# Kernel tuning notes

Measured on AMD Instinct MI355X. Metric: run time of the kernel, lower is better.

## Reference

```python
import jax, jax.numpy as jnp
import numpy as np

B, N, DIM = 2, 4096, 1024
HEADS, DH, W = 16, 64, 512
INNER = int(DIM * 2 * 4 / 3)  # 2730 (GEGLU FeedForward, mult=4)


def setup_inputs() -> dict:
    key = jax.random.key(0)
    ks = jax.random.split(key, 6)
    rn = lambda k, shape, sc: jax.random.normal(k, shape, jnp.float32) * sc
    return {
        "x": rn(ks[0], (B, N, DIM), 1.0),
        "ln1_w": jnp.ones((DIM,), jnp.float32),
        "ln1_b": jnp.zeros((DIM,), jnp.float32),
        "w_qkv": rn(ks[1], (DIM, 3 * HEADS * DH), 0.02),
        "w_out": rn(ks[2], (HEADS * DH, DIM), 0.02),
        "ln2_w": jnp.ones((DIM,), jnp.float32),
        "w_ff1": rn(ks[3], (DIM, 2 * INNER), 0.02),
        "w_ff2": rn(ks[4], (INNER, DIM), 0.02),
    }


def _layernorm(x, w, b=None, eps=1e-5):
    m = x.mean(-1, keepdims=True)
    v = x.var(-1, keepdims=True)
    y = (x - m) * jax.lax.rsqrt(v + eps) * w
    return y + b if b is not None else y


def _rotary_freqs(n, d):
    inv = 1.0 / (10000.0 ** (jnp.arange(0, d, 2, dtype=jnp.float32) / d))
    f = jnp.arange(n, dtype=jnp.float32)[:, None] * inv[None, :]  # [n, d/2]
    return jnp.concatenate([f, f], axis=-1)  # [n, d]


def _rotate_half(x):
    x1, x2 = jnp.split(x, 2, axis=-1)
    return jnp.concatenate([-x2, x1], axis=-1)


def _apply_rotary(x, freqs):
    return x * jnp.cos(freqs) + _rotate_half(x) * jnp.sin(freqs)


def reference(x, ln1_w, ln1_b, w_qkv, w_out, ln2_w, w_ff1, w_ff2):
    # ---- LocalMHA (prenorm, causal windowed attention, look_backward=1) ----
    h = _layernorm(x, ln1_w, ln1_b)
    qkv = h @ w_qkv  # [b, n, 3*h*d]
    q, k, v = jnp.split(qkv, 3, axis=-1)
    to_heads = lambda t: t.reshape(B, N, HEADS, DH).transpose(0, 2, 1, 3)  # [b,h,n,d]
    q, k, v = map(to_heads, (q, k, v))

    freqs = _rotary_freqs(N, DH)  # [n, d]
    q = _apply_rotary(q, freqs)
    k = _apply_rotary(k, freqs)
    q = q * (DH ** -0.5)

    nw = N // W
    bq = q.reshape(B, HEADS, nw, W, DH)
    bk = k.reshape(B, HEADS, nw, W, DH)
    bv = v.reshape(B, HEADS, nw, W, DH)

    def look_back(t):  # prepend previous window (zeros for first window)
        prev = jnp.concatenate([jnp.zeros_like(t[:, :, :1]), t[:, :, :-1]], axis=2)
        return jnp.concatenate([prev, t], axis=3)  # [b,h,nw,2w,d]

    kk, vv = look_back(bk), look_back(bv)

    tq = jnp.arange(N).reshape(nw, W)
    tprev = jnp.concatenate([jnp.full((1, W), -1, tq.dtype), tq[:-1]], axis=0)
    tk = jnp.concatenate([tprev, tq], axis=1)  # [nw, 2w]
    mask = (tq[:, :, None] >= tk[:, None, :]) & (tk[:, None, :] >= 0)  # causal + pad

    sim = jnp.einsum('bhnqd,bhnkd->bhnqk', bq, kk)
    sim = jnp.where(mask, sim, jnp.finfo(sim.dtype).min / 2)
    attn = jax.nn.softmax(sim, axis=-1)
    o = jnp.einsum('bhnqk,bhnkd->bhnqd', attn, vv)
    o = o.reshape(B, HEADS, N, DH).transpose(0, 2, 1, 3).reshape(B, N, HEADS * DH)
    x = o @ w_out + x  # residual

    # ---- FeedForward: LN(gamma only) -> GEGLU -> Linear, residual ----
    h = _layernorm(x, ln2_w)
    u = h @ w_ff1
    a, g = jnp.split(u, 2, axis=-1)
    x = (a * jax.nn.gelu(g, approximate=False)) @ w_ff2 + x
    return x
```

## Files before the change

kernel.cpp:

```cpp
#include <hip/hip_runtime.h>
#include <stdint.h>

typedef unsigned short u16;
typedef unsigned int u32;

#define BATCH 2
#define NSEQ  4096
#define DIM   1024
#define HEADS 16
#define DH    64
#define WIN   512
#define INNER 2730
#define ROWS  8192
#define QKV_N 3072
#define FF1_N 5460
#define FF1_NP 5632
#define INNER_P 2816
#define KROT 0.28782313663f

typedef __attribute__((ext_vector_type(8))) short short8;
typedef __attribute__((ext_vector_type(4))) float float4v;

__device__ __forceinline__ float bf2f(u16 u){ union{u32 i;float f;}c; c.i=((u32)u)<<16; return c.f; }
__device__ __forceinline__ u16 f2bf(float f){ union{float f;u32 i;}c; c.f=f; u32 i=c.i;
    return (u16)((i + 0x7FFFu + ((i>>16)&1u))>>16); }

__device__ __forceinline__ float gelu_fast(float g) {
    float t = 0.7978845608f * (g + 0.044715f * g * g * g);
    float th = 1.f - 2.f / (1.f + __expf(2.f * t));
    return 0.5f * g * (1.f + th);
}

__device__ __forceinline__ void gl_lds16(const u16* g, const u16* ldsbase) {
    __builtin_amdgcn_global_load_lds(
        (const __attribute__((address_space(1))) u32*)(uintptr_t)g,
        (__attribute__((address_space(3))) u32*)(uintptr_t)ldsbase,
        16, 0, 0);
}

__device__ __forceinline__ int ff1_src(int n, bool& ok) {
    int t = n >> 7, m = n & 127, j = m >> 4, l = m & 15;
    int p = t * 64 + ((j >> 1) << 4) + l;
    ok = (p < INNER);
    return (j & 1) ? (INNER + p) : p;
}

template <bool REMAP>
__global__ __launch_bounds__(256) void wtrans_kernel(const float* __restrict__ w, u16* __restrict__ wt,
                                                     int K0, int N0, int K1, int N1) {
    __shared__ float tile[32][33];
    int kt = blockIdx.x, nt = blockIdx.y;
    int tx = threadIdx.x & 31, ty = threadIdx.x >> 5;
    int nl = nt * 32 + tx;
    bool ok = (nl < N1);
    int sc = nl;
    if (REMAP) { bool v; sc = ff1_src(nl < N1 ? nl : 0, v); ok = ok && v; }
    else ok = ok && (nl < N0);
#pragma unroll
    for (int yy = 0; yy < 4; yy++) {
        int k = kt*32 + ty + yy*8;
        tile[ty+yy*8][tx] = (k < K0 && ok) ? w[(size_t)k*N0 + sc] : 0.f;
    }
    __syncthreads();
#pragma unroll
    for (int yy = 0; yy < 4; yy++) {
        int n = nt*32 + ty + yy*8, k = kt*32 + tx;
        if (n < N1 && k < K1) wt[(size_t)n*K1 + k] = f2bf(tile[tx][ty+yy*8]);
    }
}

__global__ __launch_bounds__(256) void ln_kernel(const float* __restrict__ x,
                                                 const float* __restrict__ w,
                                                 const float* __restrict__ b,
                                                 u16* __restrict__ out) {
    int row = blockIdx.x;
    const float* xr = x + (size_t)row * DIM;
    int t = threadIdx.x;
    float v[4];
    float s = 0.f, s2 = 0.f;
#pragma unroll
    for (int i = 0; i < 4; i++) {
        float f = xr[t + 256 * i];
        v[i] = f; s += f; s2 += f * f;
    }
#pragma unroll
    for (int off = 32; off; off >>= 1) { s += __shfl_xor(s, off); s2 += __shfl_xor(s2, off); }
    __shared__ float ls[10];
    int wave = t >> 6, lane = t & 63;
    if (lane == 0) { ls[wave] = s; ls[4 + wave] = s2; }
    __syncthreads();
    if (t == 0) {
        float ts  = ls[0] + ls[1] + ls[2] + ls[3];
        float ts2 = ls[4] + ls[5] + ls[6] + ls[7];
        float mean = ts * (1.f / DIM);
        float var  = ts2 * (1.f / DIM) - mean * mean;
        ls[8] = mean; ls[9] = 1.f / sqrtf(var + 1e-5f);
    }
    __syncthreads();
    float mean = ls[8], inv = ls[9];
    u16* orow = out + (size_t)row * DIM;
#pragma unroll
    for (int i = 0; i < 4; i++) {
        int c = t + 256 * i;
        float y = (v[i] - mean) * inv * w[c];
        if (b) y += b[c];
        orow[c] = f2bf(y);
    }
}

template <int MODE>
__global__ __launch_bounds__(512, 2) void gemm256(const u16* __restrict__ A,
                                                  const u16* __restrict__ Bt,
                                                  void* __restrict__ Cv,
                                                  int N, int K) {
    extern __shared__ u16 lds[];
    u16* Asm = lds;
    u16* Bsm = lds + 4 * 8192;
    int tiles_n = N >> 8;
    int gs  = tiles_n << 3;
    int gid = blockIdx.x / gs;
    int loc = blockIdx.x % gs;
    int tm = gid * 8 + (loc & 7);
    int tn = loc >> 3;
    int tid = threadIdx.x, wave = tid >> 6, lane = tid & 63;
    int quad = lane >> 4, l15 = lane & 15;
    int wm = wave >> 2, wn = wave & 3;
    int srow = wave * 16 + (lane >> 2);
    int sgrp = (lane & 3) ^ ((srow >> 1) & 3);
    const u16* Ag = A  + (size_t)(tm * 256 + srow) * K + sgrp * 8;
    const u16* Bg = Bt + (size_t)(tn * 256 + srow) * K + sgrp * 8;
    u16* Asw = Asm + wave * 512;
    u16* Bsw = Bsm + wave * 512;
    int rg = (l15 >> 1) & 3;
    int nk = K >> 5;

    float4v acc[8][4];
#pragma unroll
    for (int i = 0; i < 8; i++)
#pragma unroll
        for (int j = 0; j < 4; j++) acc[i][j] = (float4v){0.f, 0.f, 0.f, 0.f};

    auto stage2 = [&](int t, int h) {
        int b = t & 3;
        int k0 = t << 5;
        if (h == 0) {
            gl_lds16(Ag + k0,                   Asw + b * 8192);
            gl_lds16(Ag + (size_t)128 * K + k0, Asw + b * 8192 + 4096);
        } else {
            gl_lds16(Bg + k0,                   Bsw + b * 8192);
            gl_lds16(Bg + (size_t)128 * K + k0, Bsw + b * 8192 + 4096);
        }
    };
    auto ldsA = [&](int t, int i) -> short8 {
        const u16* Ab = Asm + (t & 3) * 8192;
        return *(const short8*)&Ab[(wm*128 + i*16 + l15) * 32 + ((quad ^ rg) * 8)];
    };
    auto ldsB = [&](int t, int j) -> short8 {
        const u16* Bb = Bsm + (t & 3) * 8192;
        return *(const short8*)&Bb[(wn*64 + j*16 + l15) * 32 + ((quad ^ rg) * 8)];
    };

    stage2(0, 0); stage2(0, 1);
    stage2(1, 0); stage2(1, 1);
    stage2(2, 0); stage2(2, 1);
    asm volatile("s_waitcnt vmcnt(8)" ::: "memory");
    __builtin_amdgcn_s_barrier();

    for (int t = 0; t < nk; ++t) {
        short8 af[8], bfr[4];
#pragma unroll
        for (int i = 0; i < 4; i++) af[i] = ldsA(t, i);
#pragma unroll
        for (int j = 0; j < 4; j++) bfr[j] = ldsB(t, j);
        if (t + 3 < nk) stage2(t + 3, 0);
        __builtin_amdgcn_s_barrier();
        asm volatile("s_waitcnt lgkmcnt(0)" ::: "memory");
        __builtin_amdgcn_sched_barrier(0);
        __builtin_amdgcn_s_setprio(1);
#pragma unroll
        for (int i = 0; i < 4; i++)
#pragma unroll
            for (int j = 0; j < 4; j++)
                acc[i][j] = __builtin_amdgcn_mfma_f32_16x16x32_bf16(af[i], bfr[j], acc[i][j], 0, 0, 0);
        __builtin_amdgcn_s_setprio(0);
        __builtin_amdgcn_s_barrier();
#pragma unroll
        for (int i = 4; i < 8; i++) af[i] = ldsA(t, i);
        if (t + 3 < nk) stage2(t + 3, 1);
        __builtin_amdgcn_s_barrier();
        asm volatile("s_waitcnt lgkmcnt(0)" ::: "memory");
        __builtin_amdgcn_sched_barrier(0);
        __builtin_amdgcn_s_setprio(1);
#pragma unroll
        for (int i = 4; i < 8; i++)
#pragma unroll
            for (int j = 0; j < 4; j++)
                acc[i][j] = __builtin_amdgcn_mfma_f32_16x16x32_bf16(af[i], bfr[j], acc[i][j], 0, 0, 0);
        __builtin_amdgcn_s_setprio(0);
        if (t < nk - 1) {
            if (t < nk - 3)       asm volatile("s_waitcnt vmcnt(8)" ::: "memory");
            else if (t == nk - 3) asm volatile("s_waitcnt vmcnt(4)" ::: "memory");
            else                  asm volatile("s_waitcnt vmcnt(0)" ::: "memory");
            __builtin_amdgcn_s_barrier();
        }
    }

    if (MODE == 2) {
        u16* C = (u16*)Cv;
        int sector = tn >> 2;
        if (sector < 2) {
            float inv0 = __expf(-(float)l15 * KROT);
            float inv1 = __expf(-(float)(l15 + 16) * KROT);
            float sc = (sector == 0) ? 0.125f : 1.0f;
#pragma unroll
            for (int i = 0; i < 8; i++) {
#pragma unroll
                for (int r = 0; r < 4; r++) {
                    int row = tm*256 + wm*128 + i*16 + quad*4 + r;
                    float fn = (float)(row & (NSEQ - 1));
                    float s0, c0, s1, c1;
                    __sincosf(fn * inv0, &s0, &c0);
                    __sincosf(fn * inv1, &s1, &c1);
                    float a0 = acc[i][0][r], a1 = acc[i][1][r];
                    float a2 = acc[i][2][r], a3 = acc[i][3][r];
                    size_t base = (size_t)row * N + tn*256 + wn*64 + l15;
                    C[base]      = f2bf((a0*c0 - a2*s0) * sc);
                    C[base + 16] = f2bf((a1*c1 - a3*s1) * sc);
                    C[base + 32] = f2bf((a2*c0 + a0*s0) * sc);
                    C[base + 48] = f2bf((a3*c1 + a1*s1) * sc);
                }
            }
        } else {
#pragma unroll
            for (int i = 0; i < 8; i++)
#pragma unroll
                for (int r = 0; r < 4; r++) {
                    size_t base = (size_t)(tm*256 + wm*128 + i*16 + quad*4 + r) * N + tn*256 + wn*64 + l15;
#pragma unroll
                    for (int j = 0; j < 4; j++) C[base + j*16] = f2bf(acc[i][j][r]);
                }
        }
        return;
    }
    if (MODE == 3) {
        u16* ag = (u16*)Cv;
        int t128 = tn * 2 + (wn >> 1);
        int cb = t128 * 64 + (wn & 1) * 32;
#pragma unroll
        for (int i = 0; i < 8; i++) {
#pragma unroll
            for (int r = 0; r < 4; r++) {
                size_t row = (size_t)(tm*256 + wm*128 + i*16 + quad*4 + r);
#pragma unroll
                for (int jp = 0; jp < 2; jp++) {
                    float a = acc[i][2*jp][r];
                    float g = acc[i][2*jp+1][r];
                    int col = cb + jp*16 + l15;
                    ag[row * INNER_P + col] = f2bf(a * gelu_fast(g));
                }
            }
        }
        return;
    }
}

template <int MODE>
__global__ __launch_bounds__(256) void gemm_tile(const u16* __restrict__ A,
                                                 const u16* __restrict__ Bt,
                                                 const float* __restrict__ resid,
                                                 void* __restrict__ Cv,
                                                 int M, int N, int K) {
    __shared__ u16 As[2][128 * 32];
    __shared__ u16 Bs[2][128 * 32];
    int tiles_n = N >> 7;
    int gs  = tiles_n << 3;
    int gid = blockIdx.x / gs;
    int loc = blockIdx.x % gs;
    int tm = gid * 8 + (loc & 7);
    int tn = loc >> 3;
    int tid = threadIdx.x, wave = tid >> 6, lane = tid & 63;
    int quad = lane >> 4, l15 = lane & 15;
    int wm = wave >> 1, wn = wave & 1;
    int srow = wave * 32 + (lane >> 2);
    int sgrp = (lane & 3) ^ ((srow >> 1) & 3);
    const u16* Ag = A  + (size_t)(tm * 128 + srow) * K + sgrp * 8;
    const u16* Bg = Bt + (size_t)(tn * 128 + srow) * K + sgrp * 8;
    const u16* Alb0 = &As[0][wave * 1024];
    const u16* Blb0 = &Bs[0][wave * 1024];
    const u16* Alb1 = &As[1][wave * 1024];
    const u16* Blb1 = &Bs[1][wave * 1024];
    int rg = (l15 >> 1) & 3;
    float4v acc[4][4];
#pragma unroll
    for (int i = 0; i < 4; i++)
#pragma unroll
        for (int j = 0; j < 4; j++) acc[i][j] = (float4v){0.f, 0.f, 0.f, 0.f};

    gl_lds16(Ag,                Alb0);
    gl_lds16(Ag + (size_t)16*K, Alb0 + 512);
    gl_lds16(Bg,                Blb0);
    gl_lds16(Bg + (size_t)16*K, Blb0 + 512);
    __syncthreads();

    int nk = K >> 5;
    for (int t = 0; t < nk; ++t) {
        int buf = t & 1;
        if (t + 1 < nk) {
            int k0 = (t + 1) << 5;
            const u16* Al = buf ? Alb0 : Alb1;
            const u16* Bl = buf ? Blb0 : Blb1;
            gl_lds16(Ag + k0,                Al);
            gl_lds16(Ag + (size_t)16*K + k0, Al + 512);
            gl_lds16(Bg + k0,                Bl);
            gl_lds16(Bg + (size_t)16*K + k0, Bl + 512);
        }
        const u16* Asb = &As[buf][0];
        const u16* Bsb = &Bs[buf][0];
        short8 af[4], bf[4];
#pragma unroll
        for (int i = 0; i < 4; i++)
            af[i] = *(const short8*)&Asb[(wm*64 + i*16 + l15)*32 + ((quad ^ rg) * 8)];
#pragma unroll
        for (int j = 0; j < 4; j++)
            bf[j] = *(const short8*)&Bsb[(wn*64 + j*16 + l15)*32 + ((quad ^ rg) * 8)];
#pragma unroll
        for (int i = 0; i < 4; i++)
#pragma unroll
            for (int j = 0; j < 4; j++)
                acc[i][j] = __builtin_amdgcn_mfma_f32_16x16x32_bf16(af[i], bf[j], acc[i][j], 0, 0, 0);
        __syncthreads();
    }
#pragma unroll
    for (int i = 0; i < 4; i++) {
#pragma unroll
        for (int r = 0; r < 4; r++) {
            size_t row = (size_t)(tm*128 + wm*64 + i*16 + quad*4 + r);
#pragma unroll
            for (int j = 0; j < 4; j++) {
                int col = tn*128 + wn*64 + j*16 + l15;
                size_t idx = row * N + col;
                float v = acc[i][j][r];
                if (MODE == 1) { if (resid) v += resid[idx]; ((float*)Cv)[idx] = v; }
                else ((u16*)Cv)[idx] = f2bf(v);
            }
        }
    }
}

__global__ __launch_bounds__(256) void vtrans_kernel(const u16* __restrict__ qkv, u16* __restrict__ vt) {
    __shared__ u16 tile[64][72];
    int t = threadIdx.x;
    int n0 = (blockIdx.x & 63) * 64;
    int hh = (blockIdx.x >> 6) & 15;
    int b  = blockIdx.x >> 10;
    int r = t >> 2, cb = (t & 3) * 16;
    const u16* src = qkv + (size_t)(b * NSEQ + n0 + r) * QKV_N + 2 * DIM + hh * 64 + cb;
    uint4 v0 = *(const uint4*)(src);
    uint4 v1 = *(const uint4*)(src + 8);
    *(uint4*)&tile[r][cb]     = v0;
    *(uint4*)&tile[r][cb + 8] = v1;
    __syncthreads();
    int d = t >> 2, nb = (t & 3) * 16;
    __align__(16) u16 vals[16];
#pragma unroll
    for (int e = 0; e < 16; e++) vals[e] = tile[nb + e][d];
    u16* dst = vt + ((size_t)(b * HEADS + hh) * DH + d) * NSEQ + n0 + nb;
    *(uint4*)(dst)     = *(uint4*)&vals[0];
    *(uint4*)(dst + 8) = *(uint4*)&vals[8];
}

__global__ __launch_bounds__(256) void attn_kernel(const u16* __restrict__ qkv,
                                                   const u16* __restrict__ vt,
                                                   u16* __restrict__ o) {
    __shared__ u16 Ks[128 * 64];
    __shared__ u16 Vs[64 * 128];
    __shared__ u16 p_lds[4][16][136];
    int tid = threadIdx.x, wave = tid >> 6, lane = tid & 63;
    int quad = lane >> 4, l15 = lane & 15;
    int bi = blockIdx.x;
    int qb = bi & 7, w0 = (bi >> 3) & 7, hh = (bi >> 6) & 15, b = bi >> 10;
    int qt = qb * 4 + wave;
    int qlocal = qt * 16 + l15;
    const u16* qp = qkv + (size_t)(b*NSEQ + w0*WIN + qt*16 + l15) * QKV_N + hh*64 + quad*8;
    short8 bq0 = *(const short8*)(qp);
    short8 bq1 = *(const short8*)(qp + 32);
    int krow0 = b * NSEQ + (w0 - 1) * WIN;
    const u16* vbase = vt + (size_t)(b * HEADS + hh) * DH * NSEQ + (w0 - 1) * WIN;
    int ks_row = lane >> 3;
    int ks_g   = (lane & 7) ^ ks_row;
    int vs_row = lane >> 4;
    int vs_j0  = lane & 15;
    int swz = l15 & 7;
    float m_ = -1e30f, l_ = 0.f;
    float4v O[4] = {{0,0,0,0},{0,0,0,0},{0,0,0,0},{0,0,0,0}};
    int cstart = (w0 == 0) ? 4 : 0;
    int clast  = (512 + qb * 64 + 63) >> 7;
    u16 (*pt)[136] = p_lds[wave];
    for (int c = cstart; c <= clast; c++) {
        int kb = c * 128;
        __syncthreads();
#pragma unroll
        for (int i = 0; i < 4; i++) {
            int kloc = wave * 32 + i * 8 + ks_row;
            gl_lds16(qkv + (size_t)(krow0 + kb + kloc) * QKV_N + DIM + hh*64 + ks_g*8,
                     &Ks[(wave*32 + i*8) * 64]);
        }
#pragma unroll
        for (int i = 0; i < 4; i++) {
            int dloc = wave * 16 + i * 4 + vs_row;
            int jsrc = vs_j0 ^ (dloc & 7);
            gl_lds16(vbase + (size_t)dloc * NSEQ + kb + jsrc * 8,
                     &Vs[(wave*16 + i*4) * 128]);
        }
        __syncthreads();
        float4v s[8];
#pragma unroll
        for (int t = 0; t < 8; t++) {
            int krow = (t*16 + l15) * 64;
            short8 ka0 = *(const short8*)&Ks[krow + ((quad    ) ^ swz) * 8];
            short8 ka1 = *(const short8*)&Ks[krow + ((quad + 4) ^ swz) * 8];
            float4v st = {0.f, 0.f, 0.f, 0.f};
            st = __builtin_amdgcn_mfma_f32_16x16x32_bf16(ka0, bq0, st, 0, 0, 0);
            st = __builtin_amdgcn_mfma_f32_16x16x32_bf16(ka1, bq1, st, 0, 0, 0);
            int ck = kb + t*16 + quad*4;
#pragma unroll
            for (int r = 0; r < 4; r++)
                if (ck + r >= 512 && ck + r - 512 > qlocal) st[r] = -1e30f;
            s[t] = st;
        }
        float mc = -1e30f;
#pragma unroll
        for (int t = 0; t < 8; t++)
#pragma unroll
            for (int r = 0; r < 4; r++) mc = fmaxf(mc, s[t][r]);
        mc = fmaxf(mc, __shfl_xor(mc, 16));
        mc = fmaxf(mc, __shfl_xor(mc, 32));
        float mn = fmaxf(m_, mc);
        float alpha = __expf(m_ - mn);
        m_ = mn;
        float su = 0.f;
#pragma unroll
        for (int t = 0; t < 8; t++) {
            union { u16 h[4]; uint2 v; } pk;
#pragma unroll
            for (int r = 0; r < 4; r++) {
                float p = __expf(s[t][r] - mn);
                su += p;
                pk.h[r] = f2bf(p);
            }
            *(uint2*)&pt[l15][t*16 + quad*4] = pk.v;
        }
        su += __shfl_xor(su, 16);
        su += __shfl_xor(su, 32);
        l_ = l_ * alpha + su;
#pragma unroll
        for (int t = 0; t < 4; t++)
#pragma unroll
            for (int r = 0; r < 4; r++) O[t][r] *= alpha;
#pragma unroll
        for (int g = 0; g < 4; g++) {
            short8 pf = *(const short8*)&pt[l15][g*32 + quad*8];
#pragma unroll
            for (int t = 0; t < 4; t++) {
                short8 vf = *(const short8*)&Vs[(t*16 + l15) * 128 + ((g*4 + quad) ^ swz) * 8];
                O[t] = __builtin_amdgcn_mfma_f32_16x16x32_bf16(vf, pf, O[t], 0, 0, 0);
            }
        }
    }
    float inv = 1.f / l_;
    u16* op = o + (size_t)(b*NSEQ + w0*WIN + qt*16 + l15) * DIM + hh*64;
#pragma unroll
    for (int t = 0; t < 4; t++) {
        union { u16 h[4]; uint2 v; } pk;
#pragma unroll
        for (int r = 0; r < 4; r++) pk.h[r] = f2bf(O[t][r] * inv);
        *(uint2*)(op + t*16 + quad*4) = pk.v;
    }
}

extern "C" void kernel_launch(void* const* d_in, const int* in_sizes, int n_in,
                              void* d_out, int out_size, void* d_ws, size_t ws_size,
                              hipStream_t stream) {
    const float* x      = (const float*)d_in[0];
    const float* ln1_w  = (const float*)d_in[1];
    const float* ln1_b  = (const float*)d_in[2];
    const float* w_qkv  = (const float*)d_in[3];
    const float* w_out  = (const float*)d_in[4];
    const float* ln2_w  = (const float*)d_in[5];
    const float* w_ff1  = (const float*)d_in[6];
    const float* w_ff2  = (const float*)d_in[7];
    float* out = (float*)d_out;

    static bool cfg = false;
    if (!cfg) {
        hipFuncSetAttribute((const void*)gemm256<2>, hipFuncAttributeMaxDynamicSharedMemorySize, 131072);
        hipFuncSetAttribute((const void*)gemm256<3>, hipFuncAttributeMaxDynamicSharedMemorySize, 131072);
        cfg = true;
    }

    char* ws = (char*)d_ws;
    size_t off = 0;
    auto alloc = [&](size_t bytes) { size_t o = off; off += (bytes + 255) & ~(size_t)255; return o; };
    size_t off_wqt  = alloc((size_t)QKV_N  * DIM * 2);
    size_t off_wot  = alloc((size_t)DIM    * DIM * 2);
    size_t off_wf1t = alloc((size_t)FF1_NP * DIM * 2);
    size_t off_wf2t = alloc((size_t)DIM    * INNER_P * 2);
    size_t off_h    = alloc((size_t)ROWS * DIM * 2);
    size_t sz_qkv = (size_t)ROWS * QKV_N * 2;
    size_t sz_vt  = (size_t)BATCH * HEADS * DH * NSEQ * 2;
    size_t off_qkv  = alloc(sz_qkv);
    size_t off_vt   = alloc(sz_vt);
    size_t off_o    = alloc((size_t)ROWS * DIM * 2);
    size_t off_x1   = alloc((size_t)ROWS * DIM * 4);
    size_t off_ag   = alloc((size_t)ROWS * INNER_P * 2);

    u16* wqt  = (u16*)(ws + off_wqt);
    u16* wot  = (u16*)(ws + off_wot);
    u16* wf1t = (u16*)(ws + off_wf1t);
    u16* wf2t = (u16*)(ws + off_wf2t);
    u16* h    = (u16*)(ws + off_h);
    u16* qkv  = (u16*)(ws + off_qkv);
    u16* vt   = (u16*)(ws + off_vt);
    u16* o    = (u16*)(ws + off_o);
    float* x1 = (float*)(ws + off_x1);
    u16* ag   = (u16*)(ws + off_ag);

    wtrans_kernel<false><<<dim3(32, 96),  256, 0, stream>>>(w_qkv, wqt,  DIM,   QKV_N, DIM,     QKV_N);
    wtrans_kernel<false><<<dim3(32, 32),  256, 0, stream>>>(w_out, wot,  DIM,   DIM,   DIM,     DIM);
    wtrans_kernel<true ><<<dim3(32, 176), 256, 0, stream>>>(w_ff1, wf1t, DIM,   FF1_N, DIM,     FF1_NP);
    wtrans_kernel<false><<<dim3(88, 32),  256, 0, stream>>>(w_ff2, wf2t, INNER, DIM,   INNER_P, DIM);

    ln_kernel<<<ROWS, 256, 0, stream>>>(x, ln1_w, ln1_b, h);
    gemm256<2><<<(ROWS/256) * (QKV_N/256), 512, 131072, stream>>>(h, wqt, qkv, QKV_N, DIM);
    vtrans_kernel<<<BATCH * HEADS * (NSEQ / 64), 256, 0, stream>>>(qkv, vt);
    attn_kernel<<<BATCH * HEADS * 8 * 8, 256, 0, stream>>>(qkv, vt, o);
    gemm_tile<1><<<(ROWS/128) * (DIM/128), 256, 0, stream>>>(o, wot, x, x1, ROWS, DIM, DIM);
    ln_kernel<<<ROWS, 256, 0, stream>>>(x1, ln2_w, nullptr, h);
    gemm256<3><<<(ROWS/256) * (FF1_NP/256), 512, 131072, stream>>>(h, wf1t, ag, FF1_NP, DIM);
    gemm_tile<1><<<(ROWS/128) * (DIM/128), 256, 0, stream>>>(ag, wf2t, x1, out, ROWS, DIM, INNER_P);

    (void)in_sizes; (void)n_in; (void)out_size; (void)ws_size;
}
```

Before: 544.0 us.

## Restructure GEMM pipelines and replace 128x128 residual GEMM with 256x128 triple-buffered kernel

The out-projection and FF2 GEMMs move from a double-buffered 128x128 tile kernel to a new 256x128 kernel. The new kernel triple-buffers in dynamic LDS, uses one barrier per k-step and launches 256 blocks with a grouped tile order. The big gemm256 kernel gets a PHASED template flag. The QKV GEMM now loads all fragments once per k-step with a single barrier, and the FF1 GEMM drops the mid-step barriers and lgkmcnt waits. The goal is less barrier and synchronisation overhead and more reuse per tile, at the cost of fewer blocks on the N=1024 GEMMs and possible LDS race hazards from the removed barriers.

```diff
diff --git a/kernel.cpp b/kernel.cpp
--- a/kernel.cpp
+++ b/kernel.cpp
@@ -108,7 +108,7 @@
     }
 }
 
-template <int MODE>
+template <int MODE, int PHASED>
 __global__ __launch_bounds__(512, 2) void gemm256(const u16* __restrict__ A,
                                                   const u16* __restrict__ Bt,
                                                   void* __restrict__ Cv,
@@ -163,45 +163,66 @@
     stage2(0, 0); stage2(0, 1);
     stage2(1, 0); stage2(1, 1);
     stage2(2, 0); stage2(2, 1);
-    asm volatile("s_waitcnt vmcnt(8)" ::: "memory");
-    __builtin_amdgcn_s_barrier();
-
-    for (int t = 0; t < nk; ++t) {
-        short8 af[8], bfr[4];
-#pragma unroll
-        for (int i = 0; i < 4; i++) af[i] = ldsA(t, i);
-#pragma unroll
-        for (int j = 0; j < 4; j++) bfr[j] = ldsB(t, j);
-        if (t + 3 < nk) stage2(t + 3, 0);
+
+    if (PHASED == 0) {
+        auto compute = [&](int t) {
+            short8 af[8], bfr[4];
+#pragma unroll
+            for (int i = 0; i < 8; i++) af[i] = ldsA(t, i);
+#pragma unroll
+            for (int j = 0; j < 4; j++) bfr[j] = ldsB(t, j);
+            __builtin_amdgcn_s_setprio(1);
+#pragma unroll
+            for (int i = 0; i < 8; i++)
+#pragma unroll
+                for (int j = 0; j < 4; j++)
+                    acc[i][j] = __builtin_amdgcn_mfma_f32_16x16x32_bf16(af[i], bfr[j], acc[i][j], 0, 0, 0);
+            __builtin_amdgcn_s_setprio(0);
+        };
+#define KSTEP(T, VM) \
+        asm volatile("s_waitcnt vmcnt(" #VM ")" ::: "memory"); \
+        __builtin_amdgcn_s_barrier(); \
+        __builtin_amdgcn_sched_barrier(0); \
+        compute(T); \
+        if ((T) + 3 < nk) { stage2((T) + 3, 0); stage2((T) + 3, 1); }
+        for (int t = 0; t < nk - 2; ++t) { KSTEP(t, 8); }
+        { KSTEP(nk - 2, 4); }
+        { KSTEP(nk - 1, 0); }
+#undef KSTEP
+    } else {
+        asm volatile("s_waitcnt vmcnt(8)" ::: "memory");
         __builtin_amdgcn_s_barrier();
-        asm volatile("s_waitcnt lgkmcnt(0)" ::: "memory");
-        __builtin_amdgcn_sched_barrier(0);
-        __builtin_amdgcn_s_setprio(1);
-#pragma unroll
-        for (int i = 0; i < 4; i++)
-#pragma unroll
-            for (int j = 0; j < 4; j++)
-                acc[i][j] = __builtin_amdgcn_mfma_f32_16x16x32_bf16(af[i], bfr[j], acc[i][j], 0, 0, 0);
-        __builtin_amdgcn_s_setprio(0);
-        __builtin_amdgcn_s_barrier();
-#pragma unroll
-        for (int i = 4; i < 8; i++) af[i] = ldsA(t, i);
-        if (t + 3 < nk) stage2(t + 3, 1);
-        __builtin_amdgcn_s_barrier();
-        asm volatile("s_waitcnt lgkmcnt(0)" ::: "memory");
-        __builtin_amdgcn_sched_barrier(0);
-        __builtin_amdgcn_s_setprio(1);
-#pragma unroll
-        for (int i = 4; i < 8; i++)
-#pragma unroll
-            for (int j = 0; j < 4; j++)
-                acc[i][j] = __builtin_amdgcn_mfma_f32_16x16x32_bf16(af[i], bfr[j], acc[i][j], 0, 0, 0);
-        __builtin_amdgcn_s_setprio(0);
-        if (t < nk - 1) {
-            if (t < nk - 3)       asm volatile("s_waitcnt vmcnt(8)" ::: "memory");
-            else if (t == nk - 3) asm volatile("s_waitcnt vmcnt(4)" ::: "memory");
-            else                  asm volatile("s_waitcnt vmcnt(0)" ::: "memory");
+        for (int t = 0; t < nk; ++t) {
+            short8 af[8], bfr[4];
+#pragma unroll
+            for (int i = 0; i < 4; i++) af[i] = ldsA(t, i);
+#pragma unroll
+            for (int j = 0; j < 4; j++) bfr[j] = ldsB(t, j);
+            if (t + 3 < nk) stage2(t + 3, 0);
+            __builtin_amdgcn_s_setprio(1);
+#pragma unroll
+            for (int i = 0; i < 4; i++)
+#pragma unroll
+                for (int j = 0; j < 4; j++)
+                    acc[i][j] = __builtin_amdgcn_mfma_f32_16x16x32_bf16(af[i], bfr[j], acc[i][j], 0, 0, 0);
+            __builtin_amdgcn_s_setprio(0);
             __builtin_amdgcn_s_barrier();
+#pragma unroll
+            for (int i = 4; i < 8; i++) af[i] = ldsA(t, i);
+            if (t + 3 < nk) stage2(t + 3, 1);
+            __builtin_amdgcn_s_setprio(1);
+#pragma unroll
+            for (int i = 4; i < 8; i++)
+#pragma unroll
+                for (int j = 0; j < 4; j++)
+                    acc[i][j] = __builtin_amdgcn_mfma_f32_16x16x32_bf16(af[i], bfr[j], acc[i][j], 0, 0, 0);
+            __builtin_amdgcn_s_setprio(0);
+            if (t < nk - 1) {
+                if (t < nk - 3)       asm volatile("s_waitcnt vmcnt(8)" ::: "memory");
+                else if (t == nk - 3) asm volatile("s_waitcnt vmcnt(4)" ::: "memory");
+                else                  asm volatile("s_waitcnt vmcnt(0)" ::: "memory");
+                __builtin_amdgcn_s_barrier();
+            }
         }
     }
 
@@ -264,84 +285,88 @@
     }
 }
 
-template <int MODE>
-__global__ __launch_bounds__(256) void gemm_tile(const u16* __restrict__ A,
-                                                 const u16* __restrict__ Bt,
-                                                 const float* __restrict__ resid,
-                                                 void* __restrict__ Cv,
-                                                 int M, int N, int K) {
-    __shared__ u16 As[2][128 * 32];
-    __shared__ u16 Bs[2][128 * 32];
-    int tiles_n = N >> 7;
-    int gs  = tiles_n << 3;
-    int gid = blockIdx.x / gs;
-    int loc = blockIdx.x % gs;
-    int tm = gid * 8 + (loc & 7);
-    int tn = loc >> 3;
+__global__ __launch_bounds__(256, 2) void gemm_mn128(const u16* __restrict__ A,
+                                                     const u16* __restrict__ Bt,
+                                                     const float* __restrict__ resid,
+                                                     float* __restrict__ C,
+                                                     int N, int K) {
+    extern __shared__ u16 lds[];
+    int x = blockIdx.x & 7, s5 = blockIdx.x >> 3;
+    int tm = x * 4 + (s5 & 3);
+    int tn = s5 >> 2;
     int tid = threadIdx.x, wave = tid >> 6, lane = tid & 63;
     int quad = lane >> 4, l15 = lane & 15;
     int wm = wave >> 1, wn = wave & 1;
-    int srow = wave * 32 + (lane >> 2);
-    int sgrp = (lane & 3) ^ ((srow >> 1) & 3);
-    const u16* Ag = A  + (size_t)(tm * 128 + srow) * K + sgrp * 8;
-    const u16* Bg = Bt + (size_t)(tn * 128 + srow) * K + sgrp * 8;
-    const u16* Alb0 = &As[0][wave * 1024];
-    const u16* Blb0 = &Bs[0][wave * 1024];
-    const u16* Alb1 = &As[1][wave * 1024];
-    const u16* Blb1 = &Bs[1][wave * 1024];
     int rg = (l15 >> 1) & 3;
-    float4v acc[4][4];
-#pragma unroll
-    for (int i = 0; i < 4; i++)
+    int srA = wave * 64 + (lane >> 2);
+    int srB = wave * 32 + (lane >> 2);
+    const u16* AgB = A  + (size_t)(tm * 256) * K;
+    const u16* BgB = Bt + (size_t)(tn * 128) * K;
+    int nk = K >> 5;
+
+    float4v acc[8][4];
+#pragma unroll
+    for (int i = 0; i < 8; i++)
 #pragma unroll
         for (int j = 0; j < 4; j++) acc[i][j] = (float4v){0.f, 0.f, 0.f, 0.f};
 
-    gl_lds16(Ag,                Alb0);
-    gl_lds16(Ag + (size_t)16*K, Alb0 + 512);
-    gl_lds16(Bg,                Blb0);
-    gl_lds16(Bg + (size_t)16*K, Blb0 + 512);
-    __syncthreads();
-
-    int nk = K >> 5;
+    auto stage = [&](int t) {
+        int s = t % 3;
+        int k0 = t << 5;
+        u16* As = lds + s * 12288;
+        u16* Bs = lds + s * 12288 + 8192;
+#pragma unroll
+        for (int q = 0; q < 4; q++) {
+            int row = srA + q * 16;
+            int g = (lane & 3) ^ ((row >> 1) & 3);
+            gl_lds16(AgB + (size_t)row * K + k0 + g * 8, As + wave * 2048 + q * 512);
+        }
+#pragma unroll
+        for (int q = 0; q < 2; q++) {
+            int row = srB + q * 16;
+            int g = (lane & 3) ^ ((row >> 1) & 3);
+            gl_lds16(BgB + (size_t)row * K + k0 + g * 8, Bs + wave * 1024 + q * 512);
+        }
+    };
+
+    stage(0); stage(1);
     for (int t = 0; t < nk; ++t) {
-        int buf = t & 1;
-        if (t + 1 < nk) {
-            int k0 = (t + 1) << 5;
-            const u16* Al = buf ? Alb0 : Alb1;
-            const u16* Bl = buf ? Blb0 : Blb1;
-            gl_lds16(Ag + k0,                Al);
-            gl_lds16(Ag + (size_t)16*K + k0, Al + 512);
-            gl_lds16(Bg + k0,                Bl);
-            gl_lds16(Bg + (size_t)16*K + k0, Bl + 512);
-        }
-        const u16* Asb = &As[buf][0];
-        const u16* Bsb = &Bs[buf][0];
-        short8 af[4], bf[4];
-#pragma unroll
-        for (int i = 0; i < 4; i++)
-            af[i] = *(const short8*)&Asb[(wm*64 + i*16 + l15)*32 + ((quad ^ rg) * 8)];
-#pragma unroll
-        for (int j = 0; j < 4; j++)
-            bf[j] = *(const short8*)&Bsb[(wn*64 + j*16 + l15)*32 + ((quad ^ rg) * 8)];
-#pragma unroll
-        for (int i = 0; i < 4; i++)
+        if (t < nk - 1) asm volatile("s_waitcnt vmcnt(6)" ::: "memory");
+        else            asm volatile("s_waitcnt vmcnt(0)" ::: "memory");
+        __builtin_amdgcn_s_barrier();
+        __builtin_amdgcn_sched_barrier(0);
+        {
+            int s = t % 3;
+            const u16* As = lds + s * 12288;
+            const u16* Bs = lds + s * 12288 + 8192;
+            short8 af[8], bfr[4];
+#pragma unroll
+            for (int i = 0; i < 8; i++)
+                af[i] = *(const short8*)&As[(wm*128 + i*16 + l15) * 32 + ((quad ^ rg) * 8)];
 #pragma unroll
             for (int j = 0; j < 4; j++)
-                acc[i][j] = __builtin_amdgcn_mfma_f32_16x16x32_bf16(af[i], bf[j], acc[i][j], 0, 0, 0);
-        __syncthreads();
-    }
-#pragma unroll
-    for (int i = 0; i < 4; i++) {
+                bfr[j] = *(const short8*)&Bs[(wn*64 + j*16 + l15) * 32 + ((quad ^ rg) * 8)];
+            __builtin_amdgcn_s_setprio(1);
+#pragma unroll
+            for (int i = 0; i < 8; i++)
+#pragma unroll
+                for (int j = 0; j < 4; j++)
+                    acc[i][j] = __builtin_amdgcn_mfma_f32_16x16x32_bf16(af[i], bfr[j], acc[i][j], 0, 0, 0);
+            __builtin_amdgcn_s_setprio(0);
+        }
+        if (t + 2 < nk) stage(t + 2);
+    }
+
+#pragma unroll
+    for (int i = 0; i < 8; i++) {
 #pragma unroll
         for (int r = 0; r < 4; r++) {
-            size_t row = (size_t)(tm*128 + wm*64 + i*16 + quad*4 + r);
+            size_t row = (size_t)(tm*256 + wm*128 + i*16 + quad*4 + r);
 #pragma unroll
             for (int j = 0; j < 4; j++) {
                 int col = tn*128 + wn*64 + j*16 + l15;
                 size_t idx = row * N + col;
-                float v = acc[i][j][r];
-                if (MODE == 1) { if (resid) v += resid[idx]; ((float*)Cv)[idx] = v; }
-                else ((u16*)Cv)[idx] = f2bf(v);
+                C[idx] = acc[i][j][r] + resid[idx];
             }
         }
     }
@@ -493,8 +518,9 @@
 
     static bool cfg = false;
     if (!cfg) {
-        hipFuncSetAttribute((const void*)gemm256<2>, hipFuncAttributeMaxDynamicSharedMemorySize, 131072);
-        hipFuncSetAttribute((const void*)gemm256<3>, hipFuncAttributeMaxDynamicSharedMemorySize, 131072);
+        hipFuncSetAttribute((const void*)gemm256<2, 0>, hipFuncAttributeMaxDynamicSharedMemorySize, 131072);
+        hipFuncSetAttribute((const void*)gemm256<3, 1>, hipFuncAttributeMaxDynamicSharedMemorySize, 131072);
+        hipFuncSetAttribute((const void*)gemm_mn128,    hipFuncAttributeMaxDynamicSharedMemorySize, 73728);
         cfg = true;
     }
 
@@ -531,13 +557,13 @@
     wtrans_kernel<false><<<dim3(88, 32),  256, 0, stream>>>(w_ff2, wf2t, INNER, DIM,   INNER_P, DIM);
 
     ln_kernel<<<ROWS, 256, 0, stream>>>(x, ln1_w, ln1_b, h);
-    gemm256<2><<<(ROWS/256) * (QKV_N/256), 512, 131072, stream>>>(h, wqt, qkv, QKV_N, DIM);
+    gemm256<2, 0><<<(ROWS/256) * (QKV_N/256), 512, 131072, stream>>>(h, wqt, qkv, QKV_N, DIM);
     vtrans_kernel<<<BATCH * HEADS * (NSEQ / 64), 256, 0, stream>>>(qkv, vt);
     attn_kernel<<<BATCH * HEADS * 8 * 8, 256, 0, stream>>>(qkv, vt, o);
-    gemm_tile<1><<<(ROWS/128) * (DIM/128), 256, 0, stream>>>(o, wot, x, x1, ROWS, DIM, DIM);
+    gemm_mn128<<<256, 256, 73728, stream>>>(o, wot, x, x1, DIM, DIM);
     ln_kernel<<<ROWS, 256, 0, stream>>>(x1, ln2_w, nullptr, h);
-    gemm256<3><<<(ROWS/256) * (FF1_NP/256), 512, 131072, stream>>>(h, wf1t, ag, FF1_NP, DIM);
-    gemm_tile<1><<<(ROWS/128) * (DIM/128), 256, 0, stream>>>(ag, wf2t, x1, out, ROWS, DIM, INNER_P);
+    gemm256<3, 1><<<(ROWS/256) * (FF1_NP/256), 512, 131072, stream>>>(h, wf1t, ag, FF1_NP, DIM);
+    gemm_mn128<<<256, 256, 73728, stream>>>(ag, wf2t, x1, out, DIM, INNER_P);
 
     (void)in_sizes; (void)n_in; (void)out_size; (void)ws_size;
 }
```

After: 527.4 us. 1.03x faster.
